# Performance work log

Hardware: AMD Instinct MI355X
Metric: run time of the kernel (lower is better)

## Reference

```python
import jax, jax.numpy as jnp
import numpy as np

D_MODEL, D_K, D_V, N_HEADS, D_FF = 1024, 64, 64, 16, 2736
EPS_NORM = 1e-12   # F.normalize eps
EPS_RMS = 1e-6     # RMSNorm eps


def _rmsnorm(x, g):
    return x * jax.lax.rsqrt(jnp.mean(x * x, axis=-1, keepdims=True) + EPS_RMS) * g


def _l2norm(x):
    n = jnp.sqrt(jnp.sum(x * x, axis=-1, keepdims=True))
    return x / jnp.maximum(n, EPS_NORM)


def setup_inputs() -> dict:
    key = jax.random.key(0)
    ks = jax.random.split(key, 10)
    B, T = 2, 1024
    s_in = 0.1 / np.sqrt(D_MODEL)   # xavier-like small init, gain 0.1
    s_ff = 0.1 / np.sqrt(D_FF)
    return {
        "x": jax.random.normal(ks[0], (B, T, D_MODEL), jnp.float32),
        "Wq": jax.random.normal(ks[1], (D_MODEL, N_HEADS * D_K), jnp.float32) * s_in,
        "Wk": jax.random.normal(ks[2], (D_MODEL, N_HEADS * D_K), jnp.float32) * s_in,
        "Wv": jax.random.normal(ks[3], (D_MODEL, N_HEADS * D_V), jnp.float32) * s_in,
        "Wg": jax.random.normal(ks[4], (D_MODEL, N_HEADS * D_K), jnp.float32) * s_in,
        "Wo": jax.random.normal(ks[5], (N_HEADS * D_V, D_MODEL), jnp.float32) * s_in,
        "w1": jax.random.normal(ks[6], (D_MODEL, D_FF), jnp.float32) * s_in,
        "w2": jax.random.normal(ks[7], (D_MODEL, D_FF), jnp.float32) * s_in,
        "w3": jax.random.normal(ks[8], (D_FF, D_MODEL), jnp.float32) * s_ff,
        "g_attn": jnp.ones((D_MODEL,), jnp.float32),
        "g_ffn": jnp.ones((D_MODEL,), jnp.float32),
    }


def _gla(h, Wq, Wk, Wv, Wg, Wo):
    B, T, _ = h.shape
    q = _l2norm((h @ Wq).reshape(B, T, N_HEADS, D_K))
    k = _l2norm((h @ Wk).reshape(B, T, N_HEADS, D_K))
    v = (h @ Wv).reshape(B, T, N_HEADS, D_V)
    alpha = jax.nn.sigmoid(h @ Wg).reshape(B, T, N_HEADS, D_K)

    def step(S, inp):
        a_t, k_t, v_t, q_t = inp                       # [B,H,dk],[B,H,dk],[B,H,dv],[B,H,dk]
        S = a_t[..., None] * S + k_t[..., None] * v_t[..., None, :]   # [B,H,dk,dv]
        o_t = jnp.einsum('bhkv,bhk->bhv', S, q_t)
        return S, o_t

    S0 = jnp.zeros((B, N_HEADS, D_K, D_V), h.dtype)
    xs = (jnp.swapaxes(alpha, 0, 1), jnp.swapaxes(k, 0, 1),
          jnp.swapaxes(v, 0, 1), jnp.swapaxes(q, 0, 1))  # time-major [T,B,H,*]
    _, o = jax.lax.scan(step, S0, xs)                    # o: [T,B,H,dv]
    o = jnp.swapaxes(o, 0, 1).reshape(B, T, N_HEADS * D_V)
    return o @ Wo


def reference(x, Wq, Wk, Wv, Wg, Wo, w1, w2, w3, g_attn, g_ffn):
    # Pre-LN GLA block: x -> Norm -> GLA -> +res -> Norm -> SwiGLU -> +res
    h = _rmsnorm(x, g_attn)
    x = x + _gla(h, Wq, Wk, Wv, Wg, Wo)
    h = _rmsnorm(x, g_ffn)
    ffn = (jax.nn.silu(h @ w1) * (h @ w2)) @ w3
    return x + ffn
```

## Files before the change

### kernel.cpp

```cpp
#include <hip/hip_runtime.h>

typedef unsigned short ushort_t;
typedef unsigned int uint32;
typedef short short8 __attribute__((ext_vector_type(8)));
typedef float f32x4 __attribute__((ext_vector_type(4)));

#define MROWS 2048
#define DMODEL 1024
#define NH 16
#define DFF 2736
#define DFFP 2752
#define NBH 32

__device__ __forceinline__ float b2f(ushort_t u) {
  return __builtin_bit_cast(float, ((uint32)u) << 16);
}
__device__ __forceinline__ ushort_t f2b(float f) {
  uint32 u = __builtin_bit_cast(uint32, f);
  return (ushort_t)((u + 0x7FFFu + ((u >> 16) & 1u)) >> 16);
}
__device__ __forceinline__ float san(float v) {
  uint32 u = __builtin_bit_cast(uint32, v);
  return (((u >> 23) & 0xFFu) == 0xFFu) ? 0.0f : v;
}
__device__ __forceinline__ float sclamp(float v, float lim) {
  return fminf(fmaxf(san(v), -lim), lim);
}

typedef const __attribute__((address_space(1))) unsigned int* gas_ptr;
typedef __attribute__((address_space(3))) unsigned int* las_ptr;
__device__ __forceinline__ void gl_lds16(const void* g, void* l) {
  __builtin_amdgcn_global_load_lds((gas_ptr)g, (las_ptr)l, 16, 0, 0);
}

__global__ __launch_bounds__(256) void rmsnorm_kernel(
    const float* __restrict__ x, const float* __restrict__ g,
    ushort_t* __restrict__ out) {
  int row = blockIdx.x;
  int tid = threadIdx.x;
  size_t base = (size_t)row * DMODEL;
  int c0 = tid * 4;
  float4 t = *(const float4*)(x + base + c0);
  float v[4] = {t.x, t.y, t.z, t.w};
  float s = v[0]*v[0] + v[1]*v[1] + v[2]*v[2] + v[3]*v[3];
  for (int off = 32; off > 0; off >>= 1) s += __shfl_xor(s, off);
  __shared__ float red[4];
  int wave = tid >> 6, lane = tid & 63;
  if (lane == 0) red[wave] = s;
  __syncthreads();
  if (tid == 0) {
    float tt = red[0] + red[1] + red[2] + red[3];
    red[0] = rsqrtf(tt * (1.0f / DMODEL) + 1e-6f);
  }
  __syncthreads();
  float sc = red[0];
  float4 gg = *(const float4*)(g + c0);
  float gv[4] = {gg.x, gg.y, gg.z, gg.w};
  for (int j = 0; j < 4; ++j)
    out[base + c0 + j] = f2b(sclamp(v[j] * sc * gv[j], 1e4f));
}

__global__ __launch_bounds__(256) void transpose_kernel(
    const float* __restrict__ S0, const float* __restrict__ S1,
    const float* __restrict__ S2, const float* __restrict__ S3,
    ushort_t* __restrict__ dst, int K, int N, int Kpad, int Npad) {
  const float* src = (blockIdx.z == 0) ? S0 : (blockIdx.z == 1) ? S1
                   : (blockIdx.z == 2) ? S2 : S3;
  ushort_t* d = dst + (size_t)blockIdx.z * Npad * Kpad;
  __shared__ ushort_t tile[32][33];
  int tx = threadIdx.x & 31, ty = threadIdx.x >> 5;
  int n0 = blockIdx.x * 32, k0 = blockIdx.y * 32;
  #pragma unroll
  for (int i = 0; i < 4; ++i) {
    int k = k0 + ty + i * 8, n = n0 + tx;
    float v = (k < K && n < N) ? src[(size_t)k * N + n] : 0.0f;
    tile[ty + i * 8][tx] = f2b(v);
  }
  __syncthreads();
  #pragma unroll
  for (int i = 0; i < 4; ++i) {
    int r = ty + i * 8;
    d[(size_t)(n0 + r) * Kpad + k0 + tx] = tile[tx][r];
  }
}

__global__ __launch_bounds__(256) void transpose5_kernel(
    const float* __restrict__ S0, const float* __restrict__ S1,
    const float* __restrict__ S2, const float* __restrict__ S3,
    const float* __restrict__ S4,
    ushort_t* __restrict__ dA, ushort_t* __restrict__ dB) {
  int z = blockIdx.z;
  const float* src = (z == 0) ? S0 : (z == 1) ? S1 : (z == 2) ? S2
                   : (z == 3) ? S3 : S4;
  ushort_t* d = (z < 4) ? (dA + (size_t)z * 1024 * 1024) : dB;
  __shared__ ushort_t tile[32][33];
  int tx = threadIdx.x & 31, ty = threadIdx.x >> 5;
  int n0 = blockIdx.x * 32, k0 = blockIdx.y * 32;
  #pragma unroll
  for (int i = 0; i < 4; ++i)
    tile[ty + i * 8][tx] = f2b(src[(size_t)(k0 + ty + i * 8) * 1024 + n0 + tx]);
  __syncthreads();
  #pragma unroll
  for (int i = 0; i < 4; ++i) {
    int r = ty + i * 8;
    d[(size_t)(n0 + r) * 1024 + k0 + tx] = tile[tx][r];
  }
}

__global__ __launch_bounds__(256) void transpose_ffn_kernel(
    const float* __restrict__ w1, const float* __restrict__ w2,
    const float* __restrict__ w3,
    ushort_t* __restrict__ dW12, ushort_t* __restrict__ dW3) {
  int z = blockIdx.z;
  const float* src; ushort_t* d; int K, N, Kpad, Npad;
  if (z < 2) {
    src = z ? w2 : w1; d = dW12 + (size_t)z * DFFP * 1024;
    K = 1024; N = DFF; Kpad = 1024; Npad = DFFP;
  } else {
    src = w3; d = dW3;
    K = DFF; N = 1024; Kpad = DFFP; Npad = 1024;
  }
  int n0 = blockIdx.x * 32, k0 = blockIdx.y * 32;
  if (n0 >= Npad || k0 >= Kpad) return;
  __shared__ ushort_t tile[32][33];
  int tx = threadIdx.x & 31, ty = threadIdx.x >> 5;
  #pragma unroll
  for (int i = 0; i < 4; ++i) {
    int k = k0 + ty + i * 8, n = n0 + tx;
    float v = (k < K && n < N) ? src[(size_t)k * N + n] : 0.0f;
    tile[ty + i * 8][tx] = f2b(v);
  }
  __syncthreads();
  #pragma unroll
  for (int i = 0; i < 4; ++i) {
    int r = ty + i * 8;
    d[(size_t)(n0 + r) * Kpad + k0 + tx] = tile[tx][r];
  }
}

template<int MODE, int BM, int BN, int NB, int MINB>
__global__ __launch_bounds__(256, MINB) void gemm_kernel(
    const ushort_t* __restrict__ A, int lda,
    const ushort_t* __restrict__ Bt, int ldb, size_t boff, int K,
    float* __restrict__ outf, ushort_t* __restrict__ outb, int ldc,
    const float* __restrict__ resf) {
  constexpr int WM = BM / 2, WN = BN / 2;
  constexpr int MF = WM / 16, FN = WN / 16;
  __shared__ __align__(16) ushort_t As0[BM * 64];
  __shared__ __align__(16) ushort_t As1[BM * 64];
  __shared__ __align__(16) ushort_t Bs0[NB][BN * 64];
  __shared__ __align__(16) ushort_t Bs1[NB][BN * 64];
  int tid = threadIdx.x;
  int wave = tid >> 6, lane = tid & 63;
  int nwg = gridDim.x * gridDim.y;
  int orig = blockIdx.y * gridDim.x + blockIdx.x;
  int swz = (orig & 7) * (nwg >> 3) + (orig >> 3);
  int n0 = (swz / gridDim.y) * BN, m0 = (swz % gridDim.y) * BM;
  int wm = (wave >> 1) * WM, wn = (wave & 1) * WN;
  int arow = lane >> 3;
  int scol = (((lane & 7) ^ arow) & 7) * 8;
  int fm = lane & 15, fk = (lane >> 4) * 8;
  int xsw = (fm & 7) * 8;
  f32x4 zero = {0.f, 0.f, 0.f, 0.f};
  f32x4 acc[MF][FN];
  f32x4 acc2[NB == 2 ? MF : 1][NB == 2 ? FN : 1];
  #pragma unroll
  for (int i = 0; i < MF; ++i)
    #pragma unroll
    for (int j = 0; j < FN; ++j) {
      acc[i][j] = zero;
      if (NB == 2) acc2[i][j] = zero;
    }
  int nK = K >> 6;
  auto stage = [&](ushort_t (&Ad)[BM * 64], ushort_t (&Bd)[NB][BN * 64],
                   int kt) {
    int k0 = kt << 6;
    #pragma unroll
    for (int i = 0; i < BM / 32; ++i) {
      int g = i * 4 + wave;
      gl_lds16(A + (size_t)(m0 + g * 8 + arow) * lda + k0 + scol, &Ad[g * 512]);
    }
    #pragma unroll
    for (int nb = 0; nb < NB; ++nb)
      #pragma unroll
      for (int i = 0; i < BN / 32; ++i) {
        int g = i * 4 + wave;
        gl_lds16(Bt + nb * boff + (size_t)(n0 + g * 8 + arow) * ldb + k0 + scol,
                 &Bd[nb][g * 512]);
      }
  };
  auto compute = [&](const ushort_t (&Ad)[BM * 64],
                     const ushort_t (&Bd)[NB][BN * 64]) {
    #pragma unroll
    for (int kk = 0; kk < 64; kk += 32) {
      short8 a[MF];
      #pragma unroll
      for (int fi = 0; fi < MF; ++fi)
        a[fi] = *(const short8*)
            &Ad[(wm + fi * 16 + fm) * 64 + ((kk + fk) ^ xsw)];
      #pragma unroll
      for (int fj = 0; fj < FN; ++fj) {
        short8 b = *(const short8*)
            &Bd[0][(wn + fj * 16 + fm) * 64 + ((kk + fk) ^ xsw)];
        #pragma unroll
        for (int fi = 0; fi < MF; ++fi)
          acc[fi][fj] =
              __builtin_amdgcn_mfma_f32_16x16x32_bf16(a[fi], b, acc[fi][fj], 0, 0, 0);
        if (NB == 2) {
          short8 b2 = *(const short8*)
              &Bd[1][(wn + fj * 16 + fm) * 64 + ((kk + fk) ^ xsw)];
          #pragma unroll
          for (int fi = 0; fi < MF; ++fi)
            acc2[fi][fj] =
                __builtin_amdgcn_mfma_f32_16x16x32_bf16(a[fi], b2, acc2[fi][fj], 0, 0, 0);
        }
      }
    }
  };
  stage(As0, Bs0, 0);
  __syncthreads();
  int t = 0;
  for (;;) {
    if (t + 1 < nK) stage(As1, Bs1, t + 1);
    compute(As0, Bs0);
    __syncthreads();
    if (++t == nK) break;
    if (t + 1 < nK) stage(As0, Bs0, t + 1);
    compute(As1, Bs1);
    __syncthreads();
    if (++t == nK) break;
  }
  int rbase = m0 + wm + ((lane >> 4) << 2);
  #pragma unroll
  for (int fi = 0; fi < MF; ++fi)
    #pragma unroll
    for (int fj = 0; fj < FN; ++fj) {
      int col = n0 + wn + fj * 16 + fm;
      #pragma unroll
      for (int reg = 0; reg < 4; ++reg) {
        int row = rbase + fi * 16 + reg;
        float v = acc[fi][fj][reg];
        size_t oidx = (size_t)row * ldc + col;
        if (MODE == 0) {
          outb[oidx] = f2b(sclamp(v, 1e4f));
        } else if (MODE == 1) {
          outf[oidx] = sclamp(v, 0.25f) + resf[oidx];
        } else if (MODE == 2) {
          float y2 = sclamp(acc2[fi][fj][reg], 1e4f);
          float vc = fminf(fmaxf(san(v), -30.f), 30.f);
          float sg = vc / (1.0f + __expf(-vc));
          outb[oidx] = f2b(sclamp(sg * y2, 1e4f));
        } else {
          outf[oidx] = sclamp(v, 0.6f) + resf[oidx];
        }
      }
    }
}

template<int MODE>
__global__ __launch_bounds__(256) void gemm64_kernel(
    const ushort_t* __restrict__ A, int lda,
    const float* __restrict__ Bq, const float* __restrict__ Bk,
    const float* __restrict__ Bv, const float* __restrict__ Bg,
    int ldb, int K, int Nb,
    float* __restrict__ outf, ushort_t* __restrict__ outb, int ldc,
    const float* __restrict__ resf) {
  constexpr int NB = (MODE == 2) ? 2 : 1;
  __shared__ __align__(16) ushort_t As[64][72];
  __shared__ __align__(16) ushort_t Bs[NB][64][72];
  int tid = threadIdx.x;
  int wave = tid >> 6, lane = tid & 63;
  int m0 = blockIdx.y * 64;
  int n0 = blockIdx.x * 64;
  const float* B = Bq;
  int bcol = n0;
  f32x4 zero = {0.f, 0.f, 0.f, 0.f};
  f32x4 acc[4];
  f32x4 acc2[NB == 2 ? 4 : 1];
  for (int i = 0; i < 4; ++i) acc[i] = zero;
  if (NB == 2) for (int i = 0; i < 4; ++i) acc2[i] = zero;
  int r  = tid >> 2;
  int cb = (tid & 3) << 4;
  int fm = lane & 15;
  int fk = (lane >> 4) << 3;
  int nK = (K + 63) >> 6;
  for (int kt = 0; kt < nK; ++kt) {
    int k0 = kt << 6;
    for (int cc = 0; cc < 16; cc += 8) {
      int c = cb + cc;
      short8 val = {0,0,0,0,0,0,0,0};
      if (k0 + c + 8 <= K)
        val = *(const short8*)(A + (size_t)(m0 + r) * lda + k0 + c);
      *(short8*)&As[r][c] = val;
    }
    for (int nb = 0; nb < NB; ++nb) {
      const float* Bp = (nb == 0) ? B : Bk;
      for (int cc = 0; cc < 16; cc += 8) {
        int c = cb + cc;
        ushort_t val[8] = {0,0,0,0,0,0,0,0};
        if (k0 + r < K && bcol + c + 8 <= Nb) {
          const float* src = Bp + (size_t)(k0 + r) * ldb + bcol + c;
          float4 f0 = *(const float4*)(src);
          float4 f1 = *(const float4*)(src + 4);
          val[0] = f2b(f0.x); val[1] = f2b(f0.y);
          val[2] = f2b(f0.z); val[3] = f2b(f0.w);
          val[4] = f2b(f1.x); val[5] = f2b(f1.y);
          val[6] = f2b(f1.z); val[7] = f2b(f1.w);
        }
        for (int j = 0; j < 8; ++j) Bs[nb][c + j][r] = val[j];
      }
    }
    __syncthreads();
    for (int kk = 0; kk < 64; kk += 32) {
      short8 a = *(const short8*)&As[wave * 16 + fm][kk + fk];
      for (int nt = 0; nt < 4; ++nt) {
        short8 b = *(const short8*)&Bs[0][nt * 16 + fm][kk + fk];
        acc[nt] = __builtin_amdgcn_mfma_f32_16x16x32_bf16(a, b, acc[nt], 0, 0, 0);
        if (NB == 2) {
          short8 b2 = *(const short8*)&Bs[1][nt * 16 + fm][kk + fk];
          acc2[nt] = __builtin_amdgcn_mfma_f32_16x16x32_bf16(a, b2, acc2[nt], 0, 0, 0);
        }
      }
    }
    __syncthreads();
  }
  int rbase = m0 + wave * 16 + ((lane >> 4) << 2);
  for (int nt = 0; nt < 4; ++nt) {
    int col = n0 + nt * 16 + (lane & 15);
    for (int reg = 0; reg < 4; ++reg) {
      int row = rbase + reg;
      float v = acc[nt][reg];
      size_t oidx = (size_t)row * ldc + col;
      if (MODE == 2) {
        if (col < Nb) {
          float y2 = sclamp(acc2[nt][reg], 1e4f);
          float vc = fminf(fmaxf(san(v), -30.f), 30.f);
          float sg = vc / (1.0f + __expf(-vc));
          outb[oidx] = f2b(sclamp(sg * y2, 1e4f));
        }
      } else if (MODE == 3) {
        outf[oidx] = sclamp(v, 0.6f) + resf[oidx];
      }
    }
  }
}

__global__ __launch_bounds__(256) void prep_kernel(ushort_t* __restrict__ yq,
                                                   float* __restrict__ Bc) {
  int h = blockIdx.x, g = blockIdx.y;
  int bh = (g >> 4) * NH + h;
  int c = g & 15;
  int r0 = g * 64;
  int tid = threadIdx.x, wave = tid >> 6, lane = tid & 63;
  __shared__ float qs[64][65], ks[64][65], gs[64][65];
  for (int t = wave; t < 64; t += 4) {
    size_t rb = (size_t)(r0 + t) * 4096 + h * 64 + lane;
    float q = san(b2f(yq[rb]));
    float s = q * q;
    for (int off = 32; off > 0; off >>= 1) s += __shfl_xor(s, off);
    qs[t][lane] = q / fmaxf(sqrtf(s), 1e-12f);
    float k = san(b2f(yq[rb + 1024]));
    s = k * k;
    for (int off = 32; off > 0; off >>= 1) s += __shfl_xor(s, off);
    ks[t][lane] = k / fmaxf(sqrtf(s), 1e-12f);
    float a = fminf(fmaxf(san(b2f(yq[rb + 3072])), -30.f), 30.f);
    gs[t][lane] = 1.0f / (1.0f + __expf(-a));
  }
  __syncthreads();
  for (int j = 0; j < 16; ++j) {
    int kd = wave * 16 + j;
    float b = gs[lane][kd];
    #pragma unroll
    for (int off = 1; off < 64; off <<= 1) {
      float p = __shfl_up(b, off);
      if (lane >= off) b *= p;
    }
    b = fmaxf(b, 1e-28f);
    float inv = fminf(1.0f / b, 1e26f);
    qs[lane][kd] = sclamp(qs[lane][kd] * b, 1e30f);
    ks[lane][kd] = sclamp(ks[lane][kd] * inv, 1e30f);
    if (lane == 63) Bc[((size_t)bh * 16 + c) * 64 + kd] = b;
  }
  __syncthreads();
  for (int t = wave; t < 64; t += 4) {
    size_t rb = (size_t)(r0 + t) * 4096 + h * 64 + lane;
    yq[rb] = f2b(qs[t][lane]);
    yq[rb + 1024] = f2b(ks[t][lane]);
  }
}

__global__ __launch_bounds__(256) void ktv_kernel(
    const ushort_t* __restrict__ yq, float* __restrict__ KtV) {
  int vs = blockIdx.x, bh = blockIdx.y, c = blockIdx.z;
  int bidx = bh >> 4, h = bh & 15;
  int tid = threadIdx.x;
  int k = tid & 63, v4 = tid >> 6;
  __shared__ float kbs[64][64];
  __shared__ float vls[64][16];
  int r0 = bidx * 1024 + c * 64;
  for (int i = tid; i < 512; i += 256) {
    int t = i >> 3, k8 = (i & 7) * 8;
    short8 s8 = *(const short8*)(yq + (size_t)(r0 + t) * 4096 + 1024 + h * 64 + k8);
    float4 lo = {b2f((ushort_t)s8[0]), b2f((ushort_t)s8[1]),
                 b2f((ushort_t)s8[2]), b2f((ushort_t)s8[3])};
    float4 hi = {b2f((ushort_t)s8[4]), b2f((ushort_t)s8[5]),
                 b2f((ushort_t)s8[6]), b2f((ushort_t)s8[7])};
    *(float4*)&kbs[t][k8] = lo;
    *(float4*)&kbs[t][k8 + 4] = hi;
  }
  for (int i = tid; i < 128; i += 256) {
    int t = i >> 1, v8 = (i & 1) * 8;
    short8 s8 = *(const short8*)(yq + (size_t)(r0 + t) * 4096 + 2048 + h * 64 +
                                 vs * 16 + v8);
    float4 lo = {b2f((ushort_t)s8[0]), b2f((ushort_t)s8[1]),
                 b2f((ushort_t)s8[2]), b2f((ushort_t)s8[3])};
    float4 hi = {b2f((ushort_t)s8[4]), b2f((ushort_t)s8[5]),
                 b2f((ushort_t)s8[6]), b2f((ushort_t)s8[7])};
    *(float4*)&vls[t][v8] = lo;
    *(float4*)&vls[t][v8 + 4] = hi;
  }
  __syncthreads();
  float S0 = 0.f, S1 = 0.f, S2 = 0.f, S3 = 0.f;
  for (int t = 0; t < 64; ++t) {
    float kv = kbs[t][k];
    float4 vv = *(const float4*)&vls[t][v4 * 4];
    S0 += kv * vv.x; S1 += kv * vv.y; S2 += kv * vv.z; S3 += kv * vv.w;
  }
  size_t ob = (((size_t)bh * 16 + c) * 64 + k) * 64 + vs * 16 + v4 * 4;
  float4 st = {S0, S1, S2, S3};
  *(float4*)(KtV + ob) = st;
}

__global__ __launch_bounds__(256) void scan_kernel(
    const float* __restrict__ KtV, const float* __restrict__ Bc,
    float* __restrict__ Sbuf) {
  int q = blockIdx.x, bh = blockIdx.y;
  int tid = threadIdx.x;
  int v4 = tid & 15, kloc = tid >> 4;
  int k = q * 16 + kloc;
  float4 S = {0.f, 0.f, 0.f, 0.f};
  size_t base = ((size_t)bh * 16) * 4096 + (size_t)k * 64 + v4 * 4;
  #pragma unroll
  for (int c = 0; c < 16; ++c) {
    size_t a = base + (size_t)c * 4096;
    *(float4*)(Sbuf + a) = S;
    float4 kv = *(const float4*)(KtV + a);
    float bc = Bc[((size_t)bh * 16 + c) * 64 + k];
    S.x = sclamp((S.x + kv.x) * bc, 1e6f);
    S.y = sclamp((S.y + kv.y) * bc, 1e6f);
    S.z = sclamp((S.z + kv.z) * bc, 1e6f);
    S.w = sclamp((S.w + kv.w) * bc, 1e6f);
  }
}

__global__ __launch_bounds__(256) void state_kernel(
    const ushort_t* __restrict__ yq, const float* __restrict__ Bc,
    float* __restrict__ Sbuf) {
  int vs = blockIdx.x;
  int bh = blockIdx.y;
  int bidx = bh >> 4, h = bh & 15;
  int tid = threadIdx.x;
  int k = tid & 63, v4 = tid >> 6;
  __shared__ float kbs[64][64];
  __shared__ float vls[64][16];
  float S[4] = {0.f, 0.f, 0.f, 0.f};
  for (int c = 0; c < 16; ++c) {
    size_t sb = (((size_t)bh * 16 + c) * 64 + k) * 64 + vs * 16 + v4 * 4;
    float4 st; st.x = S[0]; st.y = S[1]; st.z = S[2]; st.w = S[3];
    *(float4*)(Sbuf + sb) = st;
    int r0 = bidx * 1024 + c * 64;
    for (int i = tid; i < 4096; i += 256) {
      int t = i >> 6, kk = i & 63;
      kbs[t][kk] = b2f(yq[(size_t)(r0 + t) * 4096 + 1024 + h * 64 + kk]);
    }
    for (int i = tid; i < 1024; i += 256) {
      int t = i >> 4, vv = i & 15;
      vls[t][vv] = b2f(yq[(size_t)(r0 + t) * 4096 + 2048 + h * 64 + vs * 16 + vv]);
    }
    __syncthreads();
    for (int t = 0; t < 64; ++t) {
      float kv = kbs[t][k];
      S[0] += kv * vls[t][v4 * 4 + 0];
      S[1] += kv * vls[t][v4 * 4 + 1];
      S[2] += kv * vls[t][v4 * 4 + 2];
      S[3] += kv * vls[t][v4 * 4 + 3];
    }
    float bc = Bc[((size_t)bh * 16 + c) * 64 + k];
    S[0] = sclamp(S[0] * bc, 1e6f); S[1] = sclamp(S[1] * bc, 1e6f);
    S[2] = sclamp(S[2] * bc, 1e6f); S[3] = sclamp(S[3] * bc, 1e6f);
    __syncthreads();
  }
}

__global__ __launch_bounds__(256) void outk_kernel(
    const ushort_t* __restrict__ yq, const float* __restrict__ Sbuf,
    ushort_t* __restrict__ o) {
  int h = blockIdx.x;
  int g = blockIdx.y;
  int bh = (g >> 4) * NH + h;
  int c = g & 15;
  int r0 = g * 64;
  int tid = threadIdx.x, wave = tid >> 6, lane = tid & 63;
  __shared__ ushort_t Qs[64][72];
  __shared__ ushort_t Kbs[64][72];
  __shared__ ushort_t Vt[64][72];
  __shared__ ushort_t St[64][72];
  __shared__ ushort_t Ps[64][72];
  for (int i = tid; i < 512; i += 256) {
    int t = i >> 3, k8 = (i & 7) * 8;
    size_t rb = (size_t)(r0 + t) * 4096 + h * 64 + k8;
    *(short8*)&Qs[t][k8]  = *(const short8*)(yq + rb);
    *(short8*)&Kbs[t][k8] = *(const short8*)(yq + rb + 1024);
    short8 v8 = *(const short8*)(yq + rb + 2048);
    #pragma unroll
    for (int j = 0; j < 8; ++j) Vt[k8 + j][t] = (ushort_t)v8[j];
  }
  size_t sbase = (((size_t)bh * 16 + c) * 64) * 64;
  for (int i = tid; i < 1024; i += 256) {
    int kd = i >> 4, v4 = (i & 15) * 4;
    float4 s4 = *(const float4*)(Sbuf + sbase + (size_t)kd * 64 + v4);
    St[v4 + 0][kd] = f2b(sclamp(s4.x, 1e6f));
    St[v4 + 1][kd] = f2b(sclamp(s4.y, 1e6f));
    St[v4 + 2][kd] = f2b(sclamp(s4.z, 1e6f));
    St[v4 + 3][kd] = f2b(sclamp(s4.w, 1e6f));
  }
  __syncthreads();
  int wm = wave * 16;
  int fm = lane & 15, fk = (lane >> 4) * 8;
  f32x4 zero = {0.f, 0.f, 0.f, 0.f};
  f32x4 oacc[4] = {zero, zero, zero, zero};
  f32x4 pacc[4] = {zero, zero, zero, zero};
  #pragma unroll
  for (int kk = 0; kk < 64; kk += 32) {
    short8 a = *(const short8*)&Qs[wm + fm][kk + fk];
    #pragma unroll
    for (int f = 0; f < 4; ++f) {
      short8 bS = *(const short8*)&St[f * 16 + fm][kk + fk];
      oacc[f] = __builtin_amdgcn_mfma_f32_16x16x32_bf16(a, bS, oacc[f], 0, 0, 0);
      short8 bK = *(const short8*)&Kbs[f * 16 + fm][kk + fk];
      pacc[f] = __builtin_amdgcn_mfma_f32_16x16x32_bf16(a, bK, pacc[f], 0, 0, 0);
    }
  }
  int prow = wm + ((lane >> 4) << 2);
  #pragma unroll
  for (int f = 0; f < 4; ++f) {
    int s = f * 16 + fm;
    #pragma unroll
    for (int reg = 0; reg < 4; ++reg) {
      float pv = (s <= prow + reg) ? pacc[f][reg] : 0.0f;
      Ps[prow + reg][s] = f2b(pv);
    }
  }
  __syncthreads();
  #pragma unroll
  for (int kk = 0; kk < 64; kk += 32) {
    short8 a = *(const short8*)&Ps[wm + fm][kk + fk];
    #pragma unroll
    for (int f = 0; f < 4; ++f) {
      short8 bV = *(const short8*)&Vt[f * 16 + fm][kk + fk];
      oacc[f] = __builtin_amdgcn_mfma_f32_16x16x32_bf16(a, bV, oacc[f], 0, 0, 0);
    }
  }
  #pragma unroll
  for (int f = 0; f < 4; ++f) {
    int v = f * 16 + fm;
    #pragma unroll
    for (int reg = 0; reg < 4; ++reg) {
      int row = prow + reg;
      o[(size_t)(r0 + row) * 1024 + h * 64 + v] = f2b(sclamp(oacc[f][reg], 100.f));
    }
  }
}

__global__ void sentinel_kernel(float* __restrict__ out, int env) {
  if (threadIdx.x == 0 && blockIdx.x == 0)
    out[0] = 1.0e6f + 1000.0f * (float)env;
}

extern "C" void kernel_launch(void* const* d_in, const int* in_sizes, int n_in,
                              void* d_out, int out_size, void* d_ws, size_t ws_size,
                              hipStream_t stream) {
  const float* x    = (const float*)d_in[0];
  const float* Wq   = (const float*)d_in[1];
  const float* Wk   = (const float*)d_in[2];
  const float* Wv   = (const float*)d_in[3];
  const float* Wg   = (const float*)d_in[4];
  const float* Wo   = (const float*)d_in[5];
  const float* w1   = (const float*)d_in[6];
  const float* w2   = (const float*)d_in[7];
  const float* w3   = (const float*)d_in[8];
  const float* gat  = (const float*)d_in[9];
  const float* gff  = (const float*)d_in[10];
  float* out = (float*)d_out;

  char* ws = (char*)d_ws;
  const size_t R0o = 0;
  const size_t R1o = (size_t)16 * 1024 * 1024;
  const size_t R2o = (size_t)20 * 1024 * 1024;
  const size_t R3o = R2o + 128 * 1024;
  const size_t R4o = R3o + (size_t)8 * 1024 * 1024;
  const size_t W12B = (size_t)2 * DFFP * 1024 * 2;
  const size_t NEED_SMALL = R4o + 4096;
  const size_t NEED_BIG   = R4o + W12B + 4096;

  ushort_t* yq     = (ushort_t*)(ws + R0o);
  ushort_t* ff     = (ushort_t*)(ws + R0o);
  ushort_t* h1     = (ushort_t*)(ws + R1o);
  ushort_t* obuf   = (ushort_t*)(ws + R1o);
  ushort_t* h2     = (ushort_t*)(ws + R1o);
  float*    Bc     = (float*)   (ws + R2o);
  ushort_t* BtQKVG = (ushort_t*)(ws + R3o);
  float*    Sbuf   = (float*)   (ws + R3o);
  float*    x2     = (float*)   (ws + R3o);
  float*    KtV    = (float*)   (ws + R4o);
  ushort_t* BtW12  = (ushort_t*)(ws + R4o);
  ushort_t* BtW3   = (ushort_t*)(ws + R4o);

  int env = 0;
  if (ws_size < NEED_SMALL) env |= 1;
  if (n_in != 11) env |= 2;
  if (in_sizes[0] != 2097152) env |= 4;
  if (n_in == 11 && (in_sizes[1] != 1048576 || in_sizes[6] != 1024 * 2736 ||
                     in_sizes[8] != 2736 * 1024 || in_sizes[9] != 1024)) env |= 8;
  if (out_size != 2097152) env |= 16;
  if (env) {
    sentinel_kernel<<<1, 64, 0, stream>>>(out, env);
    return;
  }
  bool big = (ws_size >= NEED_BIG);
  ushort_t* BtWo = big ? (ushort_t*)(ws + R4o + (size_t)8 * 1024 * 1024)
                       : (ushort_t*)(ws + R0o);

  rmsnorm_kernel<<<MROWS, 256, 0, stream>>>(x, gat, h1);
  if (big) {
    transpose5_kernel<<<dim3(32, 32, 5), 256, 0, stream>>>(
        Wq, Wk, Wv, Wg, Wo, BtQKVG, BtWo);
  } else {
    transpose_kernel<<<dim3(32, 32, 4), 256, 0, stream>>>(
        Wq, Wk, Wv, Wg, BtQKVG, 1024, 1024, 1024, 1024);
  }
  gemm_kernel<0, 128, 128, 1, 2><<<dim3(32, 16), 256, 0, stream>>>(
      h1, DMODEL, BtQKVG, DMODEL, 0, DMODEL, nullptr, yq, 4096, nullptr);
  prep_kernel<<<dim3(16, 32), 256, 0, stream>>>(yq, Bc);
  if (big) {
    ktv_kernel<<<dim3(4, 32, 16), 256, 0, stream>>>(yq, KtV);
    scan_kernel<<<dim3(4, 32), 256, 0, stream>>>(KtV, Bc, Sbuf);
  } else {
    state_kernel<<<dim3(4, 32), 256, 0, stream>>>(yq, Bc, Sbuf);
  }
  outk_kernel<<<dim3(16, 32), 256, 0, stream>>>(yq, Sbuf, obuf);
  if (!big)
    transpose_kernel<<<dim3(32, 32, 1), 256, 0, stream>>>(
        Wo, nullptr, nullptr, nullptr, BtWo, 1024, 1024, 1024, 1024);
  gemm_kernel<1, 32, 64, 1, 5><<<dim3(16, 64), 256, 0, stream>>>(
      obuf, DMODEL, BtWo, DMODEL, 0, DMODEL, x2, nullptr, DMODEL, x);
  rmsnorm_kernel<<<MROWS, 256, 0, stream>>>(x2, gff, h2);
  if (big) {
    transpose_ffn_kernel<<<dim3(86, 86, 3), 256, 0, stream>>>(
        w1, w2, w3, BtW12, BtW3);
    gemm_kernel<2, 128, 64, 2, 2><<<dim3(43, 16), 256, 0, stream>>>(
        h2, DMODEL, BtW12, DMODEL, (size_t)DFFP * 1024, DMODEL,
        nullptr, ff, DFFP, nullptr);
    gemm_kernel<3, 32, 64, 1, 5><<<dim3(16, 64), 256, 0, stream>>>(
        ff, DFFP, BtW3, DFFP, 0, DFFP, out, nullptr, DMODEL, x2);
  } else {
    gemm64_kernel<2><<<dim3(43, 32), 256, 0, stream>>>(
        h2, DMODEL, w1, w2, nullptr, nullptr, DFF, DMODEL, DFF,
        nullptr, ff, DFF, nullptr);
    gemm64_kernel<3><<<dim3(16, 32), 256, 0, stream>>>(
        ff, DFF, w3, nullptr, nullptr, nullptr, DMODEL, DFF, DMODEL,
        out, nullptr, DMODEL, x2);
  }
}
```

Baseline: 268.4 us.

## Merge norm and weight transposes into one setup kernel; fuse prep with KtV via MFMA

```diff
diff --git a/kernel.cpp b/kernel.cpp
--- a/kernel.cpp
+++ b/kernel.cpp
@@ -33,11 +33,9 @@
   __builtin_amdgcn_global_load_lds((gas_ptr)g, (las_ptr)l, 16, 0, 0);
 }
 
-__global__ __launch_bounds__(256) void rmsnorm_kernel(
+__device__ __forceinline__ void rmsnorm_body(
     const float* __restrict__ x, const float* __restrict__ g,
-    ushort_t* __restrict__ out) {
-  int row = blockIdx.x;
-  int tid = threadIdx.x;
+    ushort_t* __restrict__ out, int row, int tid) {
   size_t base = (size_t)row * DMODEL;
   int c0 = tid * 4;
   float4 t = *(const float4*)(x + base + c0);
@@ -60,6 +58,31 @@
     out[base + c0 + j] = f2b(sclamp(v[j] * sc * gv[j], 1e4f));
 }
 
+__global__ __launch_bounds__(256) void rmsnorm_kernel(
+    const float* __restrict__ x, const float* __restrict__ g,
+    ushort_t* __restrict__ out) {
+  rmsnorm_body(x, g, out, blockIdx.x, threadIdx.x);
+}
+
+__device__ __forceinline__ void transpose_tile(
+    const float* __restrict__ src, ushort_t* __restrict__ d,
+    int K, int N, int Kpad, int n0, int k0, int tid) {
+  __shared__ ushort_t tile[32][33];
+  int tx = tid & 31, ty = tid >> 5;
+  #pragma unroll
+  for (int i = 0; i < 4; ++i) {
+    int k = k0 + ty + i * 8, n = n0 + tx;
+    float v = (k < K && n < N) ? src[(size_t)k * N + n] : 0.0f;
+    tile[ty + i * 8][tx] = f2b(v);
+  }
+  __syncthreads();
+  #pragma unroll
+  for (int i = 0; i < 4; ++i) {
+    int r = ty + i * 8;
+    d[(size_t)(n0 + r) * Kpad + k0 + tx] = tile[tx][r];
+  }
+}
+
 __global__ __launch_bounds__(256) void transpose_kernel(
     const float* __restrict__ S0, const float* __restrict__ S1,
     const float* __restrict__ S2, const float* __restrict__ S3,
@@ -67,21 +90,8 @@
   const float* src = (blockIdx.z == 0) ? S0 : (blockIdx.z == 1) ? S1
                    : (blockIdx.z == 2) ? S2 : S3;
   ushort_t* d = dst + (size_t)blockIdx.z * Npad * Kpad;
-  __shared__ ushort_t tile[32][33];
-  int tx = threadIdx.x & 31, ty = threadIdx.x >> 5;
-  int n0 = blockIdx.x * 32, k0 = blockIdx.y * 32;
-  #pragma unroll
-  for (int i = 0; i < 4; ++i) {
-    int k = k0 + ty + i * 8, n = n0 + tx;
-    float v = (k < K && n < N) ? src[(size_t)k * N + n] : 0.0f;
-    tile[ty + i * 8][tx] = f2b(v);
-  }
-  __syncthreads();
-  #pragma unroll
-  for (int i = 0; i < 4; ++i) {
-    int r = ty + i * 8;
-    d[(size_t)(n0 + r) * Kpad + k0 + tx] = tile[tx][r];
-  }
+  transpose_tile(src, d, K, N, Kpad, blockIdx.x * 32, blockIdx.y * 32,
+                 threadIdx.x);
 }
 
 __global__ __launch_bounds__(256) void transpose5_kernel(
@@ -93,18 +103,8 @@
   const float* src = (z == 0) ? S0 : (z == 1) ? S1 : (z == 2) ? S2
                    : (z == 3) ? S3 : S4;
   ushort_t* d = (z < 4) ? (dA + (size_t)z * 1024 * 1024) : dB;
-  __shared__ ushort_t tile[32][33];
-  int tx = threadIdx.x & 31, ty = threadIdx.x >> 5;
-  int n0 = blockIdx.x * 32, k0 = blockIdx.y * 32;
-  #pragma unroll
-  for (int i = 0; i < 4; ++i)
-    tile[ty + i * 8][tx] = f2b(src[(size_t)(k0 + ty + i * 8) * 1024 + n0 + tx]);
-  __syncthreads();
-  #pragma unroll
-  for (int i = 0; i < 4; ++i) {
-    int r = ty + i * 8;
-    d[(size_t)(n0 + r) * 1024 + k0 + tx] = tile[tx][r];
-  }
+  transpose_tile(src, d, 1024, 1024, 1024, blockIdx.x * 32, blockIdx.y * 32,
+                 threadIdx.x);
 }
 
 __global__ __launch_bounds__(256) void transpose_ffn_kernel(
@@ -122,19 +122,45 @@
   }
   int n0 = blockIdx.x * 32, k0 = blockIdx.y * 32;
   if (n0 >= Npad || k0 >= Kpad) return;
-  __shared__ ushort_t tile[32][33];
-  int tx = threadIdx.x & 31, ty = threadIdx.x >> 5;
-  #pragma unroll
-  for (int i = 0; i < 4; ++i) {
-    int k = k0 + ty + i * 8, n = n0 + tx;
-    float v = (k < K && n < N) ? src[(size_t)k * N + n] : 0.0f;
-    tile[ty + i * 8][tx] = f2b(v);
-  }
-  __syncthreads();
-  #pragma unroll
-  for (int i = 0; i < 4; ++i) {
-    int r = ty + i * 8;
-    d[(size_t)(n0 + r) * Kpad + k0 + tx] = tile[tx][r];
+  transpose_tile(src, d, K, N, Kpad, n0, k0, threadIdx.x);
+}
+
+__global__ __launch_bounds__(256) void setup_kernel(
+    const float* __restrict__ x, const float* __restrict__ gat,
+    ushort_t* __restrict__ h1,
+    const float* __restrict__ Wq, const float* __restrict__ Wk,
+    const float* __restrict__ Wv, const float* __restrict__ Wg,
+    const float* __restrict__ Wo,
+    ushort_t* __restrict__ dQKVG, ushort_t* __restrict__ dWo,
+    const float* __restrict__ w1, const float* __restrict__ w2,
+    const float* __restrict__ w3,
+    ushort_t* __restrict__ dW12, ushort_t* __restrict__ dW3) {
+  int bid = blockIdx.x, tid = threadIdx.x;
+  if (bid < 2048) {
+    rmsnorm_body(x, gat, h1, bid, tid);
+  } else if (bid < 7168) {
+    int idx = bid - 2048;
+    int z = idx >> 10, rem = idx & 1023;
+    const float* src = (z == 0) ? Wq : (z == 1) ? Wk : (z == 2) ? Wv
+                     : (z == 3) ? Wg : Wo;
+    ushort_t* d = (z < 4) ? (dQKVG + (size_t)z * 1024 * 1024) : dWo;
+    transpose_tile(src, d, 1024, 1024, 1024, (rem & 31) * 32, (rem >> 5) * 32,
+                   tid);
+  } else {
+    int fidx = bid - 7168;
+    const float* src; ushort_t* d; int K, N, Kpad, bx, by;
+    if (fidx < 5504) {
+      int z = fidx / 2752, t = fidx % 2752;
+      src = z ? w2 : w1; d = dW12 + (size_t)z * DFFP * 1024;
+      K = 1024; N = DFF; Kpad = 1024;
+      bx = t % 86; by = t / 86;
+    } else {
+      int t2 = fidx - 5504;
+      src = w3; d = dW3;
+      K = DFF; N = 1024; Kpad = DFFP;
+      bx = t2 % 32; by = t2 / 32;
+    }
+    transpose_tile(src, d, K, N, Kpad, bx * 32, by * 32, tid);
   }
 }
 
@@ -389,46 +415,83 @@
   }
 }
 
-__global__ __launch_bounds__(256) void ktv_kernel(
-    const ushort_t* __restrict__ yq, float* __restrict__ KtV) {
-  int vs = blockIdx.x, bh = blockIdx.y, c = blockIdx.z;
-  int bidx = bh >> 4, h = bh & 15;
-  int tid = threadIdx.x;
-  int k = tid & 63, v4 = tid >> 6;
-  __shared__ float kbs[64][64];
-  __shared__ float vls[64][16];
-  int r0 = bidx * 1024 + c * 64;
+__global__ __launch_bounds__(256) void prep_ktv_kernel(
+    ushort_t* __restrict__ yq, float* __restrict__ Bc,
+    float* __restrict__ KtV) {
+  int h = blockIdx.x, g = blockIdx.y;
+  int bh = (g >> 4) * NH + h;
+  int c = g & 15;
+  int r0 = g * 64;
+  int tid = threadIdx.x, wave = tid >> 6, lane = tid & 63;
+  __shared__ float qs[64][65], ks[64][65], gs[64][65];
+  __shared__ ushort_t Kt[64][72];
+  __shared__ ushort_t Vt[64][72];
+  for (int t = wave; t < 64; t += 4) {
+    size_t rb = (size_t)(r0 + t) * 4096 + h * 64 + lane;
+    float q = san(b2f(yq[rb]));
+    float s = q * q;
+    for (int off = 32; off > 0; off >>= 1) s += __shfl_xor(s, off);
+    qs[t][lane] = q / fmaxf(sqrtf(s), 1e-12f);
+    float k = san(b2f(yq[rb + 1024]));
+    s = k * k;
+    for (int off = 32; off > 0; off >>= 1) s += __shfl_xor(s, off);
+    ks[t][lane] = k / fmaxf(sqrtf(s), 1e-12f);
+    float a = fminf(fmaxf(san(b2f(yq[rb + 3072])), -30.f), 30.f);
+    gs[t][lane] = 1.0f / (1.0f + __expf(-a));
+  }
   for (int i = tid; i < 512; i += 256) {
-    int t = i >> 3, k8 = (i & 7) * 8;
-    short8 s8 = *(const short8*)(yq + (size_t)(r0 + t) * 4096 + 1024 + h * 64 + k8);
-    float4 lo = {b2f((ushort_t)s8[0]), b2f((ushort_t)s8[1]),
-                 b2f((ushort_t)s8[2]), b2f((ushort_t)s8[3])};
-    float4 hi = {b2f((ushort_t)s8[4]), b2f((ushort_t)s8[5]),
-                 b2f((ushort_t)s8[6]), b2f((ushort_t)s8[7])};
-    *(float4*)&kbs[t][k8] = lo;
-    *(float4*)&kbs[t][k8 + 4] = hi;
-  }
-  for (int i = tid; i < 128; i += 256) {
-    int t = i >> 1, v8 = (i & 1) * 8;
-    short8 s8 = *(const short8*)(yq + (size_t)(r0 + t) * 4096 + 2048 + h * 64 +
-                                 vs * 16 + v8);
-    float4 lo = {b2f((ushort_t)s8[0]), b2f((ushort_t)s8[1]),
-                 b2f((ushort_t)s8[2]), b2f((ushort_t)s8[3])};
-    float4 hi = {b2f((ushort_t)s8[4]), b2f((ushort_t)s8[5]),
-                 b2f((ushort_t)s8[6]), b2f((ushort_t)s8[7])};
-    *(float4*)&vls[t][v8] = lo;
-    *(float4*)&vls[t][v8 + 4] = hi;
-  }
-  __syncthreads();
-  float S0 = 0.f, S1 = 0.f, S2 = 0.f, S3 = 0.f;
-  for (int t = 0; t < 64; ++t) {
-    float kv = kbs[t][k];
-    float4 vv = *(const float4*)&vls[t][v4 * 4];
-    S0 += kv * vv.x; S1 += kv * vv.y; S2 += kv * vv.z; S3 += kv * vv.w;
-  }
-  size_t ob = (((size_t)bh * 16 + c) * 64 + k) * 64 + vs * 16 + v4 * 4;
-  float4 st = {S0, S1, S2, S3};
-  *(float4*)(KtV + ob) = st;
+    int t = i >> 3, v8 = (i & 7) * 8;
+    short8 v8v = *(const short8*)(yq + (size_t)(r0 + t) * 4096 + 2048 +
+                                  h * 64 + v8);
+    #pragma unroll
+    for (int j = 0; j < 8; ++j) Vt[v8 + j][t] = (ushort_t)v8v[j];
+  }
+  __syncthreads();
+  for (int j = 0; j < 16; ++j) {
+    int kd = wave * 16 + j;
+    float b = gs[lane][kd];
+    #pragma unroll
+    for (int off = 1; off < 64; off <<= 1) {
+      float p = __shfl_up(b, off);
+      if (lane >= off) b *= p;
+    }
+    b = fmaxf(b, 1e-28f);
+    float inv = fminf(1.0f / b, 1e26f);
+    qs[lane][kd] = sclamp(qs[lane][kd] * b, 1e30f);
+    ks[lane][kd] = sclamp(ks[lane][kd] * inv, 1e30f);
+    if (lane == 63) Bc[((size_t)bh * 16 + c) * 64 + kd] = b;
+  }
+  __syncthreads();
+  for (int t = wave; t < 64; t += 4) {
+    size_t rb = (size_t)(r0 + t) * 4096 + h * 64 + lane;
+    yq[rb] = f2b(qs[t][lane]);
+    ushort_t kb = f2b(ks[t][lane]);
+    yq[rb + 1024] = kb;
+    Kt[lane][t] = kb;
+  }
+  __syncthreads();
+  int wm = wave * 16;
+  int fm = lane & 15, fk = (lane >> 4) * 8;
+  f32x4 zero = {0.f, 0.f, 0.f, 0.f};
+  f32x4 acc[4] = {zero, zero, zero, zero};
+  #pragma unroll
+  for (int kk = 0; kk < 64; kk += 32) {
+    short8 a = *(const short8*)&Kt[wm + fm][kk + fk];
+    #pragma unroll
+    for (int f = 0; f < 4; ++f) {
+      short8 b = *(const short8*)&Vt[f * 16 + fm][kk + fk];
+      acc[f] = __builtin_amdgcn_mfma_f32_16x16x32_bf16(a, b, acc[f], 0, 0, 0);
+    }
+  }
+  size_t obase = (((size_t)bh * 16 + c) * 64) * 64;
+  int krow = wm + ((lane >> 4) << 2);
+  #pragma unroll
+  for (int f = 0; f < 4; ++f) {
+    int v = f * 16 + fm;
+    #pragma unroll
+    for (int reg = 0; reg < 4; ++reg)
+      KtV[obase + (size_t)(krow + reg) * 64 + v] = acc[f][reg];
+  }
 }
 
 __global__ __launch_bounds__(256) void scan_kernel(
@@ -600,8 +663,11 @@
   const size_t R3o = R2o + 128 * 1024;
   const size_t R4o = R3o + (size_t)8 * 1024 * 1024;
   const size_t W12B = (size_t)2 * DFFP * 1024 * 2;
+  const size_t W3B  = (size_t)1024 * DFFP * 2;
+  const size_t R5o  = R4o + (size_t)16 * 1024 * 1024;
   const size_t NEED_SMALL = R4o + 4096;
   const size_t NEED_BIG   = R4o + W12B + 4096;
+  const size_t NEED_BIG2  = R5o + W12B + W3B + 4096;
 
   ushort_t* yq     = (ushort_t*)(ws + R0o);
   ushort_t* ff     = (ushort_t*)(ws + R0o);
@@ -613,8 +679,6 @@
   float*    Sbuf   = (float*)   (ws + R3o);
   float*    x2     = (float*)   (ws + R3o);
   float*    KtV    = (float*)   (ws + R4o);
-  ushort_t* BtW12  = (ushort_t*)(ws + R4o);
-  ushort_t* BtW3   = (ushort_t*)(ws + R4o);
 
   int env = 0;
   if (ws_size < NEED_SMALL) env |= 1;
@@ -627,25 +691,35 @@
     sentinel_kernel<<<1, 64, 0, stream>>>(out, env);
     return;
   }
-  bool big = (ws_size >= NEED_BIG);
+  bool big  = (ws_size >= NEED_BIG);
+  bool big2 = (ws_size >= NEED_BIG2);
   ushort_t* BtWo = big ? (ushort_t*)(ws + R4o + (size_t)8 * 1024 * 1024)
                        : (ushort_t*)(ws + R0o);
-
-  rmsnorm_kernel<<<MROWS, 256, 0, stream>>>(x, gat, h1);
-  if (big) {
-    transpose5_kernel<<<dim3(32, 32, 5), 256, 0, stream>>>(
-        Wq, Wk, Wv, Wg, Wo, BtQKVG, BtWo);
+  ushort_t* BtW12 = big2 ? (ushort_t*)(ws + R5o)
+                         : (ushort_t*)(ws + R4o);
+  ushort_t* BtW3  = big2 ? (ushort_t*)(ws + R5o + W12B)
+                         : (ushort_t*)(ws + R4o);
+
+  if (big2) {
+    setup_kernel<<<15424, 256, 0, stream>>>(
+        x, gat, h1, Wq, Wk, Wv, Wg, Wo, BtQKVG, BtWo, w1, w2, w3, BtW12, BtW3);
   } else {
-    transpose_kernel<<<dim3(32, 32, 4), 256, 0, stream>>>(
-        Wq, Wk, Wv, Wg, BtQKVG, 1024, 1024, 1024, 1024);
+    rmsnorm_kernel<<<MROWS, 256, 0, stream>>>(x, gat, h1);
+    if (big) {
+      transpose5_kernel<<<dim3(32, 32, 5), 256, 0, stream>>>(
+          Wq, Wk, Wv, Wg, Wo, BtQKVG, BtWo);
+    } else {
+      transpose_kernel<<<dim3(32, 32, 4), 256, 0, stream>>>(
+          Wq, Wk, Wv, Wg, BtQKVG, 1024, 1024, 1024, 1024);
+    }
   }
   gemm_kernel<0, 128, 128, 1, 2><<<dim3(32, 16), 256, 0, stream>>>(
       h1, DMODEL, BtQKVG, DMODEL, 0, DMODEL, nullptr, yq, 4096, nullptr);
-  prep_kernel<<<dim3(16, 32), 256, 0, stream>>>(yq, Bc);
   if (big) {
-    ktv_kernel<<<dim3(4, 32, 16), 256, 0, stream>>>(yq, KtV);
+    prep_ktv_kernel<<<dim3(16, 32), 256, 0, stream>>>(yq, Bc, KtV);
     scan_kernel<<<dim3(4, 32), 256, 0, stream>>>(KtV, Bc, Sbuf);
   } else {
+    prep_kernel<<<dim3(16, 32), 256, 0, stream>>>(yq, Bc);
     state_kernel<<<dim3(4, 32), 256, 0, stream>>>(yq, Bc, Sbuf);
   }
   outk_kernel<<<dim3(16, 32), 256, 0, stream>>>(yq, Sbuf, obuf);
@@ -655,9 +729,7 @@
   gemm_kernel<1, 32, 64, 1, 5><<<dim3(16, 64), 256, 0, stream>>>(
       obuf, DMODEL, BtWo, DMODEL, 0, DMODEL, x2, nullptr, DMODEL, x);
   rmsnorm_kernel<<<MROWS, 256, 0, stream>>>(x2, gff, h2);
-  if (big) {
-    transpose_ffn_kernel<<<dim3(86, 86, 3), 256, 0, stream>>>(
-        w1, w2, w3, BtW12, BtW3);
+  if (big2) {
     gemm_kernel<2, 128, 64, 2, 2><<<dim3(43, 16), 256, 0, stream>>>(
         h2, DMODEL, BtW12, DMODEL, (size_t)DFFP * 1024, DMODEL,
         nullptr, ff, DFFP, nullptr);
```

After: 256.8 us. -4.3%, faster.
